# Kernel tuning notes

Hardware: AMD Instinct MI355X
Metric: run time of the kernel (lower is better)

Reference implementation:

```python
import jax, jax.numpy as jnp
import numpy as np

B, H, S, D = 4, 16, 2048, 64

def setup_inputs() -> dict:
    key = jax.random.key(0)
    kq, kk, kv = jax.random.split(key, 3)
    q = jax.random.normal(kq, (B, H, S, D), dtype=jnp.float32)
    k = jax.random.normal(kk, (B, H, S, D), dtype=jnp.float32)
    v = jax.random.normal(kv, (B, H, S, D), dtype=jnp.float32)
    return {"q_tensor": q, "k_tensor": k, "v_tensor": v}

def reference(q_tensor, k_tensor, v_tensor):
    # scores: [B, H, S, S]
    inv_scale = 1.0 / jnp.sqrt(jnp.float32(k_tensor.shape[-1]))
    scores = jnp.einsum('bhqd,bhkd->bhqk', q_tensor, k_tensor) * inv_scale
    attn = jax.nn.softmax(scores, axis=-1)
    # dropout p=0.0 -> identity
    out = jnp.einsum('bhqk,bhkd->bhqd', attn, v_tensor)
    return out
```

## Files before the change

### kernel.cpp

```cpp
#include <hip/hip_runtime.h>
#include <hip/hip_bf16.h>

#define S_LEN 2048
#define D_DIM 64
#define BH 64
#define KVBLK 64
#define NKT (S_LEN / KVBLK)
#define QBLK 256
#define NWG (BH * S_LEN / QBLK)
#define TILE_ELEMS (KVBLK * D_DIM)
#define TILE_BYTES (TILE_ELEMS * 2)

typedef __bf16 bf16_t;
typedef bf16_t bf16x8 __attribute__((ext_vector_type(8)));
typedef float f32x4 __attribute__((ext_vector_type(4)));
typedef float f32x16 __attribute__((ext_vector_type(16)));

typedef const __attribute__((address_space(1))) void gvoid_t;
typedef __attribute__((address_space(3))) void lvoid_t;

__device__ __forceinline__ int swz64(int row, int col) {
  return (row << 6) + (col ^ ((row & 7) << 3));
}

union W4 { unsigned u[4]; bf16x8 v; };
union PK { bf16_t h[2]; unsigned u; };

__global__ __launch_bounds__(256)
void preconv(const float* __restrict__ K, const float* __restrict__ V,
             bf16_t* __restrict__ Kws, bf16_t* __restrict__ Vws) {
  const int tile = blockIdx.x;
  const int bh = tile >> 5, kt = tile & 31;
  const size_t base = (size_t)bh * S_LEN * D_DIM + (size_t)kt * KVBLK * D_DIM;
  const int tid = threadIdx.x;
  bf16_t* ko = Kws + (size_t)tile * TILE_ELEMS;
  bf16_t* vo = Vws + (size_t)tile * TILE_ELEMS;

  const int krow = tid >> 2, kcb = tid & 3;
  const float* ks = K + base + (size_t)krow * D_DIM + kcb * 16;
  f32x4 kr[4];
#pragma unroll
  for (int i = 0; i < 4; ++i) kr[i] = *(const f32x4*)(ks + i * 4);
#pragma unroll
  for (int half = 0; half < 2; ++half) {
    bf16x8 f;
#pragma unroll
    for (int j = 0; j < 4; ++j) {
      f[j]     = (bf16_t)kr[half * 2][j];
      f[4 + j] = (bf16_t)kr[half * 2 + 1][j];
    }
    *(bf16x8*)&ko[swz64(krow, kcb * 16 + half * 8)] = f;
  }

  const int vkp = tid & 31, vdb = tid >> 5;
  const int vk0 = vkp * 2;
  const int vcol = (((vk0 >> 2) ^ (vk0 >> 3)) & 1) ? (vk0 ^ 12) : vk0;
  const float* vs = V + base + (size_t)vk0 * D_DIM + vdb * 8;
  f32x4 vr[4];
  vr[0] = *(const f32x4*)vs;           vr[1] = *(const f32x4*)(vs + 4);
  vr[2] = *(const f32x4*)(vs + D_DIM); vr[3] = *(const f32x4*)(vs + D_DIM + 4);
#pragma unroll
  for (int j = 0; j < 8; ++j) {
    PK p;
    p.h[0] = (bf16_t)((j < 4) ? vr[0][j] : vr[1][j - 4]);
    p.h[1] = (bf16_t)((j < 4) ? vr[2][j] : vr[3][j - 4]);
    *(unsigned*)&vo[swz64(vdb * 8 + j, vcol)] = p.u;
  }
}

__global__ __launch_bounds__(256)
void sdpa_fwd_reg(const float* __restrict__ Q, const bf16_t* __restrict__ Kws,
                  const bf16_t* __restrict__ Vws, float* __restrict__ O) {
  __shared__ bf16_t Klds[2][TILE_ELEMS];
  __shared__ bf16_t Vlds[2][TILE_ELEMS];

  const int bid = blockIdx.x;
  const int lb  = (bid & 7) * (NWG / 8) + (bid >> 3);
  const int bx  = lb & 7;
  const int bh  = lb >> 3;

  const int tid  = threadIdx.x;
  const int wave = tid >> 6;
  const int lane = tid & 63;
  const int lq   = lane & 31;
  const int h    = lane >> 5;

  const size_t base = (size_t)bh * S_LEN * D_DIM;
  const int q0 = bx * QBLK + wave * 64;
  const float qscale = 0.125f * 1.44269504089f;

  bf16x8 qf[2][4];
#pragma unroll
  for (int g = 0; g < 2; ++g) {
    const float* qp = Q + base + (size_t)(q0 + g * 32 + lq) * D_DIM + h * 8;
#pragma unroll
    for (int c = 0; c < 4; ++c) {
      f32x4 a = *(const f32x4*)(qp + c * 16);
      f32x4 b = *(const f32x4*)(qp + c * 16 + 4);
      bf16x8 f;
#pragma unroll
      for (int j = 0; j < 4; ++j) {
        f[j]     = (bf16_t)(a[j] * qscale);
        f[4 + j] = (bf16_t)(b[j] * qscale);
      }
      qf[g][c] = f;
    }
  }

  const char* kg = (const char*)(Kws + (size_t)(bh * NKT) * TILE_ELEMS)
                   + wave * 2048 + lane * 16;
  const char* vg = (const char*)(Vws + (size_t)(bh * NKT) * TILE_ELEMS)
                   + wave * 2048 + lane * 16;

  auto issue = [&](int kt, int buf) {
    const char* ksrc = kg + (size_t)kt * TILE_BYTES;
    const char* vsrc = vg + (size_t)kt * TILE_BYTES;
    char* kd = (char*)&Klds[buf][0] + wave * 2048;
    char* vd = (char*)&Vlds[buf][0] + wave * 2048;
    __builtin_amdgcn_global_load_lds((gvoid_t*)ksrc,          (lvoid_t*)kd,          16, 0, 0);
    __builtin_amdgcn_global_load_lds((gvoid_t*)(ksrc + 1024), (lvoid_t*)(kd + 1024), 16, 0, 0);
    __builtin_amdgcn_global_load_lds((gvoid_t*)vsrc,          (lvoid_t*)vd,          16, 0, 0);
    __builtin_amdgcn_global_load_lds((gvoid_t*)(vsrc + 1024), (lvoid_t*)(vd + 1024), 16, 0, 0);
  };

  f32x16 accA0 = {}, accA1 = {};
  f32x16 accB0 = {}, accB1 = {};
  float lpA = 0.f, lpB = 0.f;

  issue(0, 0);

#pragma unroll 1
  for (int t = 0; t < NKT; ++t) {
    __builtin_amdgcn_s_barrier();
    __builtin_amdgcn_sched_barrier(0);
    if (t + 1 < NKT) issue(t + 1, (t + 1) & 1);

    const bf16_t* Kb = Klds[t & 1];
    const bf16_t* Vb = Vlds[t & 1];

#pragma unroll
    for (int role = 0; role < 2; ++role) {
      bf16x8 kf[4];
#pragma unroll
      for (int c = 0; c < 4; ++c)
        kf[c] = *(const bf16x8*)&Kb[swz64(role * 32 + lq, c * 16 + h * 8)];

      f32x16 sA = {}, sB = {};
      __builtin_amdgcn_s_setprio(1);
#pragma unroll
      for (int c = 0; c < 4; ++c) {
        sA = __builtin_amdgcn_mfma_f32_32x32x16_bf16(kf[c], qf[0][c], sA, 0, 0, 0);
        sB = __builtin_amdgcn_mfma_f32_32x32x16_bf16(kf[c], qf[1][c], sB, 0, 0, 0);
      }
      __builtin_amdgcn_s_setprio(0);

      bf16x8 vf[4];
#pragma unroll
      for (int j = 0; j < 2; ++j) {
        const int kc = role * 2 + j;
        vf[j * 2]     = *(const bf16x8*)&Vb[swz64(lq,      kc * 16 + h * 8)];
        vf[j * 2 + 1] = *(const bf16x8*)&Vb[swz64(32 + lq, kc * 16 + h * 8)];
      }

#pragma unroll
      for (int r = 0; r < 16; ++r) {
        sA[r] = __builtin_amdgcn_exp2f(sA[r]);
        sB[r] = __builtin_amdgcn_exp2f(sB[r]);
      }
      lpA += ((sA[0]+sA[1])+(sA[2]+sA[3])) + ((sA[4]+sA[5])+(sA[6]+sA[7]))
           + ((sA[8]+sA[9])+(sA[10]+sA[11])) + ((sA[12]+sA[13])+(sA[14]+sA[15]));
      lpB += ((sB[0]+sB[1])+(sB[2]+sB[3])) + ((sB[4]+sB[5])+(sB[6]+sB[7]))
           + ((sB[8]+sB[9])+(sB[10]+sB[11])) + ((sB[12]+sB[13])+(sB[14]+sB[15]));

      bf16x8 pA[2], pB[2];
#pragma unroll
      for (int j = 0; j < 2; ++j) {
        W4 wa, wb;
#pragma unroll
        for (int i = 0; i < 4; ++i) {
          PK a, b;
          a.h[0] = (bf16_t)sA[j * 8 + 2 * i]; a.h[1] = (bf16_t)sA[j * 8 + 2 * i + 1];
          b.h[0] = (bf16_t)sB[j * 8 + 2 * i]; b.h[1] = (bf16_t)sB[j * 8 + 2 * i + 1];
          wa.u[i] = a.u; wb.u[i] = b.u;
        }
        pA[j] = wa.v; pB[j] = wb.v;
      }

      __builtin_amdgcn_s_setprio(1);
#pragma unroll
      for (int j = 0; j < 2; ++j) {
        accA0 = __builtin_amdgcn_mfma_f32_32x32x16_bf16(vf[j*2],   pA[j], accA0, 0, 0, 0);
        accA1 = __builtin_amdgcn_mfma_f32_32x32x16_bf16(vf[j*2+1], pA[j], accA1, 0, 0, 0);
        accB0 = __builtin_amdgcn_mfma_f32_32x32x16_bf16(vf[j*2],   pB[j], accB0, 0, 0, 0);
        accB1 = __builtin_amdgcn_mfma_f32_32x32x16_bf16(vf[j*2+1], pB[j], accB1, 0, 0, 0);
      }
      __builtin_amdgcn_s_setprio(0);
    }

    asm volatile("s_waitcnt vmcnt(0)" ::: "memory");
  }

  float lA = lpA + __shfl_xor(lpA, 32, 64);
  float lB = lpB + __shfl_xor(lpB, 32, 64);
  float iA = 1.0f / lA, iB = 1.0f / lB;
  float* opA = O + base + (size_t)(q0 + lq) * D_DIM;
  float* opB = O + base + (size_t)(q0 + 32 + lq) * D_DIM;
#pragma unroll
  for (int r = 0; r < 16; ++r) {
    int d = (r & 3) + 8 * (r >> 2) + 4 * h;
    opA[d]      = accA0[r] * iA;
    opA[32 + d] = accA1[r] * iA;
    opB[d]      = accB0[r] * iB;
    opB[32 + d] = accB1[r] * iB;
  }
}

__global__ __launch_bounds__(256, 2)
void sdpa_fwd_fb(const float* __restrict__ Q, const float* __restrict__ K,
                 const float* __restrict__ V, float* __restrict__ O) {
  __shared__ bf16_t Klds[2][KVBLK * D_DIM];
  __shared__ bf16_t VTlds[2][D_DIM * KVBLK];

  const int bid = blockIdx.x;
  const int lb  = (bid & 7) * 128 + (bid >> 3);
  const int bx  = lb & 15;
  const int bh  = lb >> 4;

  const int tid  = threadIdx.x;
  const int wave = tid >> 6;
  const int lane = tid & 63;
  const int lq   = lane & 31;
  const int h    = lane >> 5;

  const size_t base = (size_t)bh * S_LEN * D_DIM;
  const int q0 = bx * 128 + wave * 32;
  const float qscale = 0.125f * 1.44269504089f;

  bf16x8 qf[4];
  {
    const float* qp = Q + base + (size_t)(q0 + lq) * D_DIM + h * 8;
#pragma unroll
    for (int c = 0; c < 4; ++c) {
      f32x4 a = *(const f32x4*)(qp + c * 16);
      f32x4 b = *(const f32x4*)(qp + c * 16 + 4);
      bf16x8 f;
#pragma unroll
      for (int j = 0; j < 4; ++j) {
        f[j]     = (bf16_t)(a[j] * qscale);
        f[4 + j] = (bf16_t)(b[j] * qscale);
      }
      qf[c] = f;
    }
  }

  const int krow = tid >> 2, kcb = tid & 3;
  const int vkp = tid & 31, vdb = tid >> 5;
  const int vk0 = vkp * 2;
  const int vcol = (((vk0 >> 2) ^ (vk0 >> 3)) & 1) ? (vk0 ^ 12) : vk0;

  f32x4 kr[4], vr[4];

  auto issue = [&](int kt) {
    const float* ks = K + base + (size_t)(kt * KVBLK + krow) * D_DIM + kcb * 16;
#pragma unroll
    for (int i = 0; i < 4; ++i) kr[i] = *(const f32x4*)(ks + i * 4);
    const float* vs = V + base + (size_t)(kt * KVBLK + vk0) * D_DIM + vdb * 8;
    vr[0] = *(const f32x4*)vs;           vr[1] = *(const f32x4*)(vs + 4);
    vr[2] = *(const f32x4*)(vs + D_DIM); vr[3] = *(const f32x4*)(vs + D_DIM + 4);
  };

  auto stage = [&](int buf) {
#pragma unroll
    for (int half = 0; half < 2; ++half) {
      bf16x8 f;
#pragma unroll
      for (int j = 0; j < 4; ++j) {
        f[j]     = (bf16_t)kr[half * 2][j];
        f[4 + j] = (bf16_t)kr[half * 2 + 1][j];
      }
      *(bf16x8*)&Klds[buf][swz64(krow, kcb * 16 + half * 8)] = f;
    }
#pragma unroll
    for (int j = 0; j < 8; ++j) {
      PK p;
      p.h[0] = (bf16_t)((j < 4) ? vr[0][j] : vr[1][j - 4]);
      p.h[1] = (bf16_t)((j < 4) ? vr[2][j] : vr[3][j - 4]);
      *(unsigned*)&VTlds[buf][swz64(vdb * 8 + j, vcol)] = p.u;
    }
  };

  f32x16 acc0 = {}, acc1 = {};
  float m = -1e30f, l = 0.f;

  issue(0);
  stage(0);
  __syncthreads();

  for (int kt = 0; kt < NKT; ++kt) {
    const int cur = kt & 1;
    if (kt + 1 < NKT) issue(kt + 1);

    const bf16_t* Kb = Klds[cur];
    const bf16_t* Vb = VTlds[cur];

    f32x16 st0 = {}, st1 = {};
    __builtin_amdgcn_s_setprio(1);
#pragma unroll
    for (int c = 0; c < 4; ++c) {
      bf16x8 kf0 = *(const bf16x8*)&Kb[swz64(lq, c * 16 + h * 8)];
      bf16x8 kf1 = *(const bf16x8*)&Kb[swz64(32 + lq, c * 16 + h * 8)];
      st0 = __builtin_amdgcn_mfma_f32_32x32x16_bf16(kf0, qf[c], st0, 0, 0, 0);
      st1 = __builtin_amdgcn_mfma_f32_32x32x16_bf16(kf1, qf[c], st1, 0, 0, 0);
    }
    __builtin_amdgcn_s_setprio(0);

    float t16[16];
#pragma unroll
    for (int r = 0; r < 16; ++r) t16[r] = fmaxf(st0[r], st1[r]);
#pragma unroll
    for (int off = 8; off > 0; off >>= 1)
#pragma unroll
      for (int i = 0; i < off; ++i) t16[i] = fmaxf(t16[i], t16[i + off]);
    float pmax = fmaxf(t16[0], __shfl_xor(t16[0], 32, 64));

    if (!__all(pmax - m <= 8.0f)) {
      float mn = fmaxf(m, pmax);
      float al = exp2f(m - mn);
      m = mn; l *= al;
#pragma unroll
      for (int r = 0; r < 16; ++r) { acc0[r] *= al; acc1[r] *= al; }
    }

#pragma unroll
    for (int r = 0; r < 16; ++r) {
      st0[r] = exp2f(st0[r] - m);
      st1[r] = exp2f(st1[r] - m);
    }
    float sm[16];
#pragma unroll
    for (int r = 0; r < 16; ++r) sm[r] = st0[r] + st1[r];
#pragma unroll
    for (int off = 8; off > 0; off >>= 1)
#pragma unroll
      for (int i = 0; i < off; ++i) sm[i] += sm[i + off];
    l += sm[0] + __shfl_xor(sm[0], 32, 64);

    bf16x8 pf[4];
#pragma unroll
    for (int s2 = 0; s2 < 2; ++s2) {
      W4 w0, w1;
#pragma unroll
      for (int i = 0; i < 4; ++i) {
        PK a, b;
        a.h[0] = (bf16_t)(s2 ? st1[2 * i]     : st0[2 * i]);
        a.h[1] = (bf16_t)(s2 ? st1[2 * i + 1] : st0[2 * i + 1]);
        b.h[0] = (bf16_t)(s2 ? st1[8 + 2 * i]     : st0[8 + 2 * i]);
        b.h[1] = (bf16_t)(s2 ? st1[8 + 2 * i + 1] : st0[8 + 2 * i + 1]);
        w0.u[i] = a.u; w1.u[i] = b.u;
      }
      pf[s2 * 2] = w0.v; pf[s2 * 2 + 1] = w1.v;
    }

    __builtin_amdgcn_s_setprio(1);
#pragma unroll
    for (int kc = 0; kc < 4; ++kc) {
      bf16x8 vf0 = *(const bf16x8*)&Vb[swz64(lq, kc * 16 + h * 8)];
      bf16x8 vf1 = *(const bf16x8*)&Vb[swz64(32 + lq, kc * 16 + h * 8)];
      acc0 = __builtin_amdgcn_mfma_f32_32x32x16_bf16(vf0, pf[kc], acc0, 0, 0, 0);
      acc1 = __builtin_amdgcn_mfma_f32_32x32x16_bf16(vf1, pf[kc], acc1, 0, 0, 0);
    }
    __builtin_amdgcn_s_setprio(0);

    if (kt + 1 < NKT) stage(cur ^ 1);
    __syncthreads();
  }

  float invl = 1.0f / l;
  float* op = O + base + (size_t)(q0 + lq) * D_DIM;
#pragma unroll
  for (int r = 0; r < 16; ++r) {
    int d = (r & 3) + 8 * (r >> 2) + 4 * h;
    op[d]      = acc0[r] * invl;
    op[32 + d] = acc1[r] * invl;
  }
}

extern "C" void kernel_launch(void* const* d_in, const int* in_sizes, int n_in,
                              void* d_out, int out_size, void* d_ws, size_t ws_size,
                              hipStream_t stream) {
  const float* q = (const float*)d_in[0];
  const float* k = (const float*)d_in[1];
  const float* v = (const float*)d_in[2];
  float* o = (float*)d_out;

  const size_t tile_cnt = (size_t)BH * NKT;
  const size_t need = 2 * tile_cnt * TILE_ELEMS * sizeof(bf16_t);

  if (ws_size >= need) {
    bf16_t* kws = (bf16_t*)d_ws;
    bf16_t* vws = kws + tile_cnt * TILE_ELEMS;
    preconv<<<(int)tile_cnt, 256, 0, stream>>>(k, v, kws, vws);
    sdpa_fwd_reg<<<NWG, 256, 0, stream>>>(q, kws, vws, o);
  } else {
    sdpa_fwd_fb<<<1024, 256, 0, stream>>>(q, k, v, o);
  }
}
```

Measured before the change: 103.7 us.

## Split KV sequence across two workgroups and merge partial outputs

Adds a split-K (flash-decoding style) variant of the register kernel. Each query block's KV range is divided in two, doubling the grid from 512 to 1024 workgroups so more CUs are occupied on the 256-CU device. Each half writes unnormalised partial numerators and row sums to workspace, and a separate merge kernel combines them. This costs an extra launch plus roughly 64MB of fp32 partial traffic. The fallback kernel also drops its setprio hints. The merge relies on the existing fixed-max scheme, so no max rescale is needed.

```diff
diff --git a/kernel.cpp b/kernel.cpp
--- a/kernel.cpp
+++ b/kernel.cpp
@@ -7,7 +7,6 @@
 #define KVBLK 64
 #define NKT (S_LEN / KVBLK)
 #define QBLK 256
-#define NWG (BH * S_LEN / QBLK)
 #define TILE_ELEMS (KVBLK * D_DIM)
 #define TILE_BYTES (TILE_ELEMS * 2)
 
@@ -68,16 +67,22 @@
   }
 }
 
+template<int NSPLIT>
 __global__ __launch_bounds__(256)
 void sdpa_fwd_reg(const float* __restrict__ Q, const bf16_t* __restrict__ Kws,
-                  const bf16_t* __restrict__ Vws, float* __restrict__ O) {
+                  const bf16_t* __restrict__ Vws, float* __restrict__ O,
+                  float* __restrict__ Npart, float* __restrict__ Lpart) {
   __shared__ bf16_t Klds[2][TILE_ELEMS];
   __shared__ bf16_t Vlds[2][TILE_ELEMS];
 
+  constexpr int NWGT = 512 * NSPLIT;
+  constexpr int TPB  = NKT / NSPLIT;
+
   const int bid = blockIdx.x;
-  const int lb  = (bid & 7) * (NWG / 8) + (bid >> 3);
-  const int bx  = lb & 7;
-  const int bh  = lb >> 3;
+  const int lb  = (bid & 7) * (NWGT / 8) + (bid >> 3);
+  int ks, bx, bh;
+  if (NSPLIT == 2) { ks = lb & 1; bx = (lb >> 1) & 7; bh = lb >> 4; }
+  else             { ks = 0;      bx = lb & 7;        bh = lb >> 3; }
 
   const int tid  = threadIdx.x;
   const int wave = tid >> 6;
@@ -127,16 +132,17 @@
   f32x16 accB0 = {}, accB1 = {};
   float lpA = 0.f, lpB = 0.f;
 
-  issue(0, 0);
+  const int t0 = ks * TPB;
+  issue(t0, 0);
 
 #pragma unroll 1
-  for (int t = 0; t < NKT; ++t) {
+  for (int lt = 0; lt < TPB; ++lt) {
     __builtin_amdgcn_s_barrier();
     __builtin_amdgcn_sched_barrier(0);
-    if (t + 1 < NKT) issue(t + 1, (t + 1) & 1);
-
-    const bf16_t* Kb = Klds[t & 1];
-    const bf16_t* Vb = Vlds[t & 1];
+    if (lt + 1 < TPB) issue(t0 + lt + 1, (lt + 1) & 1);
+
+    const bf16_t* Kb = Klds[lt & 1];
+    const bf16_t* Vb = Vlds[lt & 1];
 
 #pragma unroll
     for (int role = 0; role < 2; ++role) {
@@ -202,17 +208,51 @@
 
   float lA = lpA + __shfl_xor(lpA, 32, 64);
   float lB = lpB + __shfl_xor(lpB, 32, 64);
-  float iA = 1.0f / lA, iB = 1.0f / lB;
-  float* opA = O + base + (size_t)(q0 + lq) * D_DIM;
-  float* opB = O + base + (size_t)(q0 + 32 + lq) * D_DIM;
-#pragma unroll
-  for (int r = 0; r < 16; ++r) {
-    int d = (r & 3) + 8 * (r >> 2) + 4 * h;
-    opA[d]      = accA0[r] * iA;
-    opA[32 + d] = accA1[r] * iA;
-    opB[d]      = accB0[r] * iB;
-    opB[32 + d] = accB1[r] * iB;
-  }
+
+  if (NSPLIT == 1) {
+    float iA = 1.0f / lA, iB = 1.0f / lB;
+    float* opA = O + base + (size_t)(q0 + lq) * D_DIM;
+    float* opB = O + base + (size_t)(q0 + 32 + lq) * D_DIM;
+#pragma unroll
+    for (int r = 0; r < 16; ++r) {
+      int d = (r & 3) + 8 * (r >> 2) + 4 * h;
+      opA[d]      = accA0[r] * iA;
+      opA[32 + d] = accA1[r] * iA;
+      opB[d]      = accB0[r] * iB;
+      opB[32 + d] = accB1[r] * iB;
+    }
+  } else {
+    float* np = Npart + ((size_t)ks * BH + bh) * S_LEN * D_DIM;
+    float* npA = np + (size_t)(q0 + lq) * D_DIM;
+    float* npB = np + (size_t)(q0 + 32 + lq) * D_DIM;
+#pragma unroll
+    for (int r = 0; r < 16; ++r) {
+      int d = (r & 3) + 8 * (r >> 2) + 4 * h;
+      npA[d]      = accA0[r];
+      npA[32 + d] = accA1[r];
+      npB[d]      = accB0[r];
+      npB[32 + d] = accB1[r];
+    }
+    float* lp = Lpart + ((size_t)ks * BH + bh) * S_LEN;
+    if (h == 0) lp[q0 + lq] = lA;
+    else        lp[q0 + 32 + lq] = lB;
+  }
+}
+
+__global__ __launch_bounds__(256)
+void merge_halves(const float* __restrict__ Npart, const float* __restrict__ Lpart,
+                  float* __restrict__ O) {
+  const size_t idx = (size_t)blockIdx.x * 256 + threadIdx.x;
+  const size_t row = idx >> 4;
+  const int f4c = (int)(idx & 15);
+  const size_t half = (size_t)BH * S_LEN * D_DIM;
+  const float* n0 = Npart + row * D_DIM + f4c * 4;
+  const float* n1 = n0 + half;
+  f32x4 a = *(const f32x4*)n0;
+  f32x4 b = *(const f32x4*)n1;
+  float l = Lpart[row] + Lpart[(size_t)BH * S_LEN + row];
+  f32x4 o = (a + b) * (1.0f / l);
+  *(f32x4*)(O + row * D_DIM + f4c * 4) = o;
 }
 
 __global__ __launch_bounds__(256, 2)
@@ -304,7 +344,6 @@
     const bf16_t* Vb = VTlds[cur];
 
     f32x16 st0 = {}, st1 = {};
-    __builtin_amdgcn_s_setprio(1);
 #pragma unroll
     for (int c = 0; c < 4; ++c) {
       bf16x8 kf0 = *(const bf16x8*)&Kb[swz64(lq, c * 16 + h * 8)];
@@ -312,7 +351,6 @@
       st0 = __builtin_amdgcn_mfma_f32_32x32x16_bf16(kf0, qf[c], st0, 0, 0, 0);
       st1 = __builtin_amdgcn_mfma_f32_32x32x16_bf16(kf1, qf[c], st1, 0, 0, 0);
     }
-    __builtin_amdgcn_s_setprio(0);
 
     float t16[16];
 #pragma unroll
@@ -361,7 +399,6 @@
       pf[s2 * 2] = w0.v; pf[s2 * 2 + 1] = w1.v;
     }
 
-    __builtin_amdgcn_s_setprio(1);
 #pragma unroll
     for (int kc = 0; kc < 4; ++kc) {
       bf16x8 vf0 = *(const bf16x8*)&Vb[swz64(lq, kc * 16 + h * 8)];
@@ -369,7 +406,6 @@
       acc0 = __builtin_amdgcn_mfma_f32_32x32x16_bf16(vf0, pf[kc], acc0, 0, 0, 0);
       acc1 = __builtin_amdgcn_mfma_f32_32x32x16_bf16(vf1, pf[kc], acc1, 0, 0, 0);
     }
-    __builtin_amdgcn_s_setprio(0);
 
     if (kt + 1 < NKT) stage(cur ^ 1);
     __syncthreads();
@@ -394,13 +430,24 @@
   float* o = (float*)d_out;
 
   const size_t tile_cnt = (size_t)BH * NKT;
-  const size_t need = 2 * tile_cnt * TILE_ELEMS * sizeof(bf16_t);
-
-  if (ws_size >= need) {
+  const size_t kv_bytes = 2 * tile_cnt * TILE_ELEMS * sizeof(bf16_t);
+  const size_t n_bytes  = 2 * (size_t)BH * S_LEN * D_DIM * 4;
+  const size_t l_bytes  = 2 * (size_t)BH * S_LEN * 4;
+  const size_t need_split = kv_bytes + n_bytes + l_bytes;
+
+  if (ws_size >= kv_bytes) {
     bf16_t* kws = (bf16_t*)d_ws;
     bf16_t* vws = kws + tile_cnt * TILE_ELEMS;
     preconv<<<(int)tile_cnt, 256, 0, stream>>>(k, v, kws, vws);
-    sdpa_fwd_reg<<<NWG, 256, 0, stream>>>(q, kws, vws, o);
+    if (ws_size >= need_split) {
+      float* npart = (float*)((char*)d_ws + kv_bytes);
+      float* lpart = (float*)((char*)d_ws + kv_bytes + n_bytes);
+      sdpa_fwd_reg<2><<<1024, 256, 0, stream>>>(q, kws, vws, o, npart, lpart);
+      const size_t f4_total = (size_t)BH * S_LEN * D_DIM / 4;
+      merge_halves<<<(int)(f4_total / 256), 256, 0, stream>>>(npart, lpart, o);
+    } else {
+      sdpa_fwd_reg<1><<<512, 256, 0, stream>>>(q, kws, vws, o, nullptr, nullptr);
+    }
   } else {
     sdpa_fwd_fb<<<1024, 256, 0, stream>>>(q, k, v, o);
   }
```

After: 121.5 us. +17.2%, slower.
